# Optimization experiments

Measured on AMD Instinct MI355X. Metric: run time of the kernel, lower is better.

Reference implementation:

```python
import jax, jax.numpy as jnp
import numpy as np

WIN = 9
EPS = 1e-05


def _box3d(x, win=WIN):
    """Sum over a win^3 box (zero-padded), equivalent to conv3d with a ones kernel.
    Implemented as three separable 1D convolutions (exact same math, O(win)/voxel)."""
    pad = win // 2
    for axis in range(3):  # spatial axes D, H, W
        kshape = [1, 1, 1, 1, 1]
        kshape[2 + axis] = win
        kern = jnp.ones(kshape, x.dtype)
        pads = [(0, 0)] * 3
        pads[axis] = (pad, pad)
        dn = jax.lax.conv_dimension_numbers(x.shape, kern.shape, ('NCDHW', 'OIDHW', 'NCDHW'))
        x = jax.lax.conv_general_dilated(x, kern, window_strides=(1, 1, 1),
                                         padding=pads, dimension_numbers=dn)
    return x


def setup_inputs() -> dict:
    key = jax.random.key(0)
    k1, k2 = jax.random.split(key)
    shape = (1, 1, 160, 192, 224)  # [N, C, D, H, W] brain-MRI-scale volume
    I = jax.random.normal(k1, shape, dtype=jnp.float32)
    J = jax.random.normal(k2, shape, dtype=jnp.float32)
    return {"I": I, "J": J}


def reference(I, J):
    win_size = WIN ** 3
    I2 = I * I
    J2 = J * J
    IJ = I * J
    I_sum = _box3d(I)
    J_sum = _box3d(J)
    I2_sum = _box3d(I2)
    J2_sum = _box3d(J2)
    IJ_sum = _box3d(IJ)
    u_I = I_sum / win_size
    u_J = J_sum / win_size
    cross = IJ_sum - u_J * I_sum - u_I * J_sum + u_I * u_J * win_size
    I_var = I2_sum - 2 * u_I * I_sum + u_I * u_I * win_size
    J_var = J2_sum - 2 * u_J * J_sum + u_J * u_J * win_size
    cc = cross * cross / (I_var * J_var + EPS)
    return -1.0 * jnp.mean(cc)
```

## Files before the change

### kernel.cpp

```cpp
#include <hip/hip_runtime.h>


#define DD 160
#define HH 192
#define WW 224
#define W4 56
#define SLICE (HH * WW)
#define S4 (SLICE / 4)
#define NVOX (DD * SLICE)
#define TW 32
#define TH 16
#define DCH 20
#define ITERS (DCH + 8)
#define NTHR 512
#define SW_RS 36
#define SW_CS (24 * SW_RS)
#define EPS 1e-5f
#define INV_WSUM (1.0f / 729.0f)

__global__ __launch_bounds__(NTHR, 4) void ncc_fused(const float* __restrict__ I,
                                                     const float* __restrict__ J,
                                                     float* __restrict__ out) {
    __shared__ float SW0[5 * SW_CS], SW1[5 * SW_CS];
    __shared__ float SH[TH * TW * 5];
    __shared__ float wred[NTHR / 64];

    const int tid = threadIdx.x;
    const int tx = tid & 31, ty = tid >> 5;
    const int wlo = blockIdx.x * TW;
    const int hlo = blockIdx.y * TH;
    const int dlo = blockIdx.z * DCH;

    const int wr = tid >> 3, wc = tid & 7;
    const int gh = hlo - 4 + wr;
    const bool hok = (gh >= 0) && (gh < HH);
    const int gf0 = (wlo >> 2) - 1 + wc;

    const int ht = tid - 192;
    const int hcol = ht & 31, hch = ht >> 5;

    const float4* Iv = (const float4*)I;
    const float4* Jv = (const float4*)J;

    auto w_stage = [&](int z, float* dst) {
        const int rowb = z * S4 + gh * W4;
        float ax[12], bx[12];
        #pragma unroll
        for (int k = 0; k < 3; ++k) {
            const int f = gf0 + k;
            float4 a = make_float4(0.f, 0.f, 0.f, 0.f);
            float4 b = make_float4(0.f, 0.f, 0.f, 0.f);
            if (hok && f >= 0 && f < W4) { a = Iv[rowb + f]; b = Jv[rowb + f]; }
            ax[4*k] = a.x; ax[4*k+1] = a.y; ax[4*k+2] = a.z; ax[4*k+3] = a.w;
            bx[4*k] = b.x; bx[4*k+1] = b.y; bx[4*k+2] = b.z; bx[4*k+3] = b.w;
        }
        float* wp = dst + wr * SW_RS + 4 * wc;
        #pragma unroll
        for (int ch = 0; ch < 5; ++ch) {
            float v[12];
            #pragma unroll
            for (int k = 0; k < 12; ++k)
                v[k] = (ch == 0) ? ax[k]
                     : (ch == 1) ? bx[k]
                     : (ch == 2) ? ax[k] * ax[k]
                     : (ch == 3) ? bx[k] * bx[k]
                     :             ax[k] * bx[k];
            float s = v[0];
            #pragma unroll
            for (int k = 1; k < 9; ++k) s += v[k];
            float4 o;
            o.x = s;
            s += v[9]  - v[0]; o.y = s;
            s += v[10] - v[1]; o.z = s;
            s += v[11] - v[2]; o.w = s;
            *(float4*)(wp + ch * SW_CS) = o;
        }
    };

    float q0[9], q1[9], q2[9], q3[9], q4[9];
    #pragma unroll
    for (int k = 0; k < 9; ++k) { q0[k]=0.f; q1[k]=0.f; q2[k]=0.f; q3[k]=0.f; q4[k]=0.f; }
    float r0=0.f, r1=0.f, r2=0.f, r3=0.f, r4=0.f;
    float acc = 0.f;

    if (tid < 192 && dlo >= 4) w_stage(dlo - 4, SW0);
    __syncthreads();

    #pragma unroll 1
    for (int g = 0; g < 4; ++g) {
        #pragma unroll
        for (int ph = 0; ph < 9; ++ph) {
            const int i = 9 * g + ph;
            const int z = dlo - 4 + i;
            const bool live = (i < ITERS);
            const bool val = live && (z >= 0) && (z < DD);
            const int par = i & 1;
            float* swR = par ? SW1 : SW0;
            float* swW = par ? SW0 : SW1;

            if (tid < 192) {
                const int zn = z + 1;
                if (i < ITERS - 1 && zn >= 0 && zn < DD) w_stage(zn, swW);
            } else if (ht < 160 && val) {
                const float* p = swR + hch * SW_CS + hcol;
                float v[24];
                #pragma unroll
                for (int r = 0; r < 24; r += 2) {
                    const float* pr = p + r * SW_RS;
                    v[r]     = pr[0];
                    v[r + 1] = pr[SW_RS];
                }
                float s = v[0];
                #pragma unroll
                for (int r = 1; r < 9; ++r) s += v[r];
                float* o = SH + hcol * 5 + hch;
                float prev = s;
                o[0] = s;
                #pragma unroll
                for (int r = 1; r < 16; ++r) {
                    prev += v[r + 8] - v[r - 1];
                    o[r * (TW * 5)] = prev;
                }
            }
            __syncthreads();

            float w0=0.f, w1=0.f, w2=0.f, w3=0.f, w4=0.f;
            if (val) {
                const float* p = SH + (ty * TW + tx) * 5;
                w0 = p[0]; w1 = p[1]; w2 = p[2]; w3 = p[3]; w4 = p[4];
            }
            r0 += w0 - q0[ph]; q0[ph] = w0;
            r1 += w1 - q1[ph]; q1[ph] = w1;
            r2 += w2 - q2[ph]; q2[ph] = w2;
            r3 += w3 - q3[ph]; q3[ph] = w3;
            r4 += w4 - q4[ph]; q4[ph] = w4;

            if (live && i >= 8) {
                float cross = r4 - r0 * r1 * INV_WSUM;
                float iv    = r2 - r0 * r0 * INV_WSUM;
                float jv    = r3 - r1 * r1 * INV_WSUM;
                acc += cross * cross * __builtin_amdgcn_rcpf(iv * jv + EPS);
            }
            __syncthreads();
        }
    }

    #pragma unroll
    for (int off = 32; off > 0; off >>= 1) acc += __shfl_down(acc, off, 64);
    if ((tid & 63) == 0) wred[tid >> 6] = acc;
    __syncthreads();
    if (tid == 0) {
        float t = 0.f;
        #pragma unroll
        for (int k = 0; k < NTHR / 64; ++k) t += wred[k];
        atomicAdd(out, t * (-1.0f / (float)NVOX));
    }
}

extern "C" void kernel_launch(void* const* d_in, const int* in_sizes, int n_in,
                              void* d_out, int out_size, void* d_ws, size_t ws_size,
                              hipStream_t stream) {
    const float* I = (const float*)d_in[0];
    const float* J = (const float*)d_in[1];
    float* out = (float*)d_out;

    hipMemsetAsync(d_out, 0, sizeof(float), stream);

    dim3 blk(NTHR, 1, 1);
    dim3 grd(WW / TW, HH / TH, DD / DCH);
    ncc_fused<<<grd, blk, 0, stream>>>(I, J, out);
}
```

Before: 138.8 us.

## Prefetch next slice into registers and resize depth chunk to fit loop

Splits the W-stage into a global load into registers and a compute/store step, so the load for slice z+2 is issued one iteration ahead and its latency overlaps the barrier and H-stage work. The depth chunk drops from 20 to 19, giving 27 iterations that fit exactly in three unrolled groups of nine instead of four groups with dead iterations. The grid is rounded up and out-of-range slices are masked. This adds register pressure from the prefetch buffers and a partial last chunk with extra halo overhead.

```diff
diff --git a/kernel.cpp b/kernel.cpp
--- a/kernel.cpp
+++ b/kernel.cpp
@@ -10,7 +10,7 @@
 #define NVOX (DD * SLICE)
 #define TW 32
 #define TH 16
-#define DCH 20
+#define DCH 19
 #define ITERS (DCH + 8)
 #define NTHR 512
 #define SW_RS 36
@@ -42,29 +42,34 @@
     const float4* Iv = (const float4*)I;
     const float4* Jv = (const float4*)J;
 
-    auto w_stage = [&](int z, float* dst) {
+    float pfa[12], pfb[12];
+
+    auto w_load = [&](int z) {
+        const bool zok = (z >= 0) && (z < DD) && hok;
         const int rowb = z * S4 + gh * W4;
-        float ax[12], bx[12];
         #pragma unroll
         for (int k = 0; k < 3; ++k) {
             const int f = gf0 + k;
             float4 a = make_float4(0.f, 0.f, 0.f, 0.f);
             float4 b = make_float4(0.f, 0.f, 0.f, 0.f);
-            if (hok && f >= 0 && f < W4) { a = Iv[rowb + f]; b = Jv[rowb + f]; }
-            ax[4*k] = a.x; ax[4*k+1] = a.y; ax[4*k+2] = a.z; ax[4*k+3] = a.w;
-            bx[4*k] = b.x; bx[4*k+1] = b.y; bx[4*k+2] = b.z; bx[4*k+3] = b.w;
+            if (zok && f >= 0 && f < W4) { a = Iv[rowb + f]; b = Jv[rowb + f]; }
+            pfa[4*k] = a.x; pfa[4*k+1] = a.y; pfa[4*k+2] = a.z; pfa[4*k+3] = a.w;
+            pfb[4*k] = b.x; pfb[4*k+1] = b.y; pfb[4*k+2] = b.z; pfb[4*k+3] = b.w;
         }
+    };
+
+    auto w_compute = [&](float* dst) {
         float* wp = dst + wr * SW_RS + 4 * wc;
         #pragma unroll
         for (int ch = 0; ch < 5; ++ch) {
             float v[12];
             #pragma unroll
             for (int k = 0; k < 12; ++k)
-                v[k] = (ch == 0) ? ax[k]
-                     : (ch == 1) ? bx[k]
-                     : (ch == 2) ? ax[k] * ax[k]
-                     : (ch == 3) ? bx[k] * bx[k]
-                     :             ax[k] * bx[k];
+                v[k] = (ch == 0) ? pfa[k]
+                     : (ch == 1) ? pfb[k]
+                     : (ch == 2) ? pfa[k] * pfa[k]
+                     : (ch == 3) ? pfb[k] * pfb[k]
+                     :             pfa[k] * pfb[k];
             float s = v[0];
             #pragma unroll
             for (int k = 1; k < 9; ++k) s += v[k];
@@ -83,24 +88,30 @@
     float r0=0.f, r1=0.f, r2=0.f, r3=0.f, r4=0.f;
     float acc = 0.f;
 
-    if (tid < 192 && dlo >= 4) w_stage(dlo - 4, SW0);
+    if (tid < 192) {
+        w_load(dlo - 4);
+        if (dlo >= 4) w_compute(SW0);
+        w_load(dlo - 3);
+    }
     __syncthreads();
 
     #pragma unroll 1
-    for (int g = 0; g < 4; ++g) {
+    for (int g = 0; g < 3; ++g) {
         #pragma unroll
         for (int ph = 0; ph < 9; ++ph) {
             const int i = 9 * g + ph;
             const int z = dlo - 4 + i;
-            const bool live = (i < ITERS);
-            const bool val = live && (z >= 0) && (z < DD);
+            const bool val = (z >= 0) && (z < DD);
             const int par = i & 1;
             float* swR = par ? SW1 : SW0;
             float* swW = par ? SW0 : SW1;
 
             if (tid < 192) {
-                const int zn = z + 1;
-                if (i < ITERS - 1 && zn >= 0 && zn < DD) w_stage(zn, swW);
+                if (i < ITERS - 1) {
+                    const int zn = z + 1;
+                    if (zn >= 0 && zn < DD) w_compute(swW);
+                    w_load(z + 2);
+                }
             } else if (ht < 160 && val) {
                 const float* p = swR + hch * SW_CS + hcol;
                 float v[24];
@@ -135,7 +146,7 @@
             r3 += w3 - q3[ph]; q3[ph] = w3;
             r4 += w4 - q4[ph]; q4[ph] = w4;
 
-            if (live && i >= 8) {
+            if (i >= 8 && (dlo + i - 8) < DD) {
                 float cross = r4 - r0 * r1 * INV_WSUM;
                 float iv    = r2 - r0 * r0 * INV_WSUM;
                 float jv    = r3 - r1 * r1 * INV_WSUM;
@@ -167,6 +178,6 @@
     hipMemsetAsync(d_out, 0, sizeof(float), stream);
 
     dim3 blk(NTHR, 1, 1);
-    dim3 grd(WW / TW, HH / TH, DD / DCH);
+    dim3 grd(WW / TW, HH / TH, (DD + DCH - 1) / DCH);
     ncc_fused<<<grd, blk, 0, stream>>>(I, J, out);
 }
```

New measurement: 137.5 us. Within noise of the previous version (-0.9%).
